# Optimization experiments

Measured on AMD Instinct MI355X. Metric: run time of the kernel, lower is better.

The kernel has to match this reference:

```python
import jax, jax.numpy as jnp
import numpy as np

N_GRAPHS = 100
BN_EPS = 1e-5
L = 4


def batch_norm(x, gamma, beta):
    # torch BatchNorm1d in training mode: biased batch statistics over the node dim
    mu = jnp.mean(x, axis=0)
    var = jnp.var(x, axis=0)
    return gamma * (x - mu) * jax.lax.rsqrt(var + BN_EPS) + beta


def setup_inputs() -> dict:
    key = jax.random.key(0)
    ks = jax.random.split(key, 24)
    N, E, IN, H, C = 50000, 600000, 128, 128, 10
    s = 0.05
    inp = {
        "h": jax.random.normal(ks[0], (N, IN), jnp.float32),
        "snorm_n": jax.random.uniform(ks[1], (N, 1), jnp.float32),
        "edge_src": jax.random.randint(ks[2], (E,), 0, N, jnp.int32),
        "edge_dst": jax.random.randint(ks[3], (E,), 0, N, jnp.int32),
        "graph_ids": jnp.sort(jax.random.randint(ks[4], (N,), 0, N_GRAPHS, jnp.int32)),
        # embedding_h
        "emb_W": jax.random.normal(ks[5], (IN, H), jnp.float32) * s,
        "emb_b": jnp.zeros((H,), jnp.float32),
        # per-layer GIN params, stacked over L layers
        "eps": jnp.zeros((L,), jnp.float32),
        "W1": jax.random.normal(ks[6], (L, H, H), jnp.float32) * s,
        "b1": jnp.zeros((L, H), jnp.float32),
        "g1": jnp.ones((L, H), jnp.float32),   # MLP internal BN gamma
        "be1": jnp.zeros((L, H), jnp.float32),  # MLP internal BN beta
        "W2": jax.random.normal(ks[7], (L, H, H), jnp.float32) * s,
        "b2": jnp.zeros((L, H), jnp.float32),
        "ga": jnp.ones((L, H), jnp.float32),    # ApplyNodeFunc BN gamma
        "ba": jnp.zeros((L, H), jnp.float32),
        "gl": jnp.ones((L, H), jnp.float32),    # GINLayer node BN gamma
        "bl": jnp.zeros((L, H), jnp.float32),
        # linears_prediction (L+1 of them)
        "pred_W": jax.random.normal(ks[8], (L + 1, H, C), jnp.float32) * s,
        "pred_b": jnp.zeros((L + 1, C), jnp.float32),
    }
    return inp


def reference(h, snorm_n, edge_src, edge_dst, graph_ids, emb_W, emb_b, eps,
              W1, b1, g1, be1, W2, b2, ga, ba, gl, bl, pred_W, pred_b):
    N = h.shape[0]
    h = h @ emb_W + emb_b  # embedding_h
    hidden_rep = [h]
    for i in range(L):
        h_in = h
        # sum-aggregate neighbor features (irregular gather + scatter-add)
        neigh = jax.ops.segment_sum(h[edge_src], edge_dst, num_segments=N)
        z = (1.0 + eps[i]) * h + neigh
        # ApplyNodeFunc: MLP (lin->BN->relu->lin) then BN then relu
        z = jax.nn.relu(batch_norm(z @ W1[i] + b1[i], g1[i], be1[i]))
        z = z @ W2[i] + b2[i]
        z = jax.nn.relu(batch_norm(z, ga[i], ba[i]))
        z = z * snorm_n                      # graph_norm
        z = batch_norm(z, gl[i], bl[i])      # batch_norm
        z = jax.nn.relu(z)
        h = h_in + z                         # residual (dropout p=0)
        hidden_rep.append(h)
    score = jnp.zeros((N_GRAPHS, pred_W.shape[-1]), h.dtype)
    for i, hr in enumerate(hidden_rep):
        pooled = jax.ops.segment_sum(hr, graph_ids, num_segments=N_GRAPHS)
        score = score + pooled @ pred_W[i] + pred_b[i]
    return score
```

## Files before the change

### kernel.cpp

```cpp
#include <hip/hip_runtime.h>

#define HD __device__ __forceinline__

static constexpr int H = 128;
static constexpr int G = 100;
static constexpr int L = 4;
static constexpr int C = 10;
static constexpr int DEGCAP = 64;

typedef __attribute__((ext_vector_type(8))) short short8;
typedef __attribute__((ext_vector_type(4))) float f32x4;

HD float bf2f(unsigned int u16) {
    return __uint_as_float(u16 << 16);
}
HD unsigned int f2bf(float f) {
    unsigned int u = __float_as_uint(f);
    u += 0x7fffu + ((u >> 16) & 1u);
    return u >> 16;
}

__global__ __launch_bounds__(256) void wprep_kernel(const float* __restrict__ embW,
                                                    const float* __restrict__ W1,
                                                    const float* __restrict__ W2,
                                                    unsigned short* __restrict__ WT,
                                                    unsigned short* __restrict__ Hb) {
    int mat = blockIdx.y;
    if (mat == 0 && blockIdx.x == 0 && threadIdx.x < 64)
        ((unsigned int*)Hb)[threadIdx.x] = 0u;
    const float* src = (mat == 0) ? embW
                     : (mat <= L) ? W1 + (size_t)(mat - 1) * H * H
                                  : W2 + (size_t)(mat - 1 - L) * H * H;
    int t = blockIdx.x * 256 + threadIdx.x;
    int col = t >> 7, k = t & 127;
    WT[(size_t)mat * H * H + col * H + k] = (unsigned short)f2bf(src[(size_t)k * H + col]);
}

__global__ void fill_kernel(const int* __restrict__ src, const int* __restrict__ dst, int E,
                            int* __restrict__ cnt, int* __restrict__ esrc) {
    int e = blockIdx.x * blockDim.x + threadIdx.x;
    if (e < E) {
        int d = dst[e];
        int pos = atomicAdd(&cnt[d], 1) & (DEGCAP - 1);
        esrc[(size_t)d * DEGCAP + pos] = src[e] + 1;
    }
}

__global__ __launch_bounds__(256) void agg_kernel(const unsigned short* __restrict__ HbZ,
                                                  const int* __restrict__ cnt,
                                                  const int* __restrict__ esrc,
                                                  const float* __restrict__ eps, int layer,
                                                  unsigned short* __restrict__ ZB, int N) {
    int node = blockIdx.x * 4 + (threadIdx.x >> 6);
    int lane = threadIdx.x & 63;
    if (node >= N) return;
    const unsigned int* H2 = (const unsigned int*)HbZ;
    float e1 = 1.0f + eps[layer];
    unsigned int hv = H2[(size_t)(node + 1) * 64 + lane];
    float ax = e1 * bf2f(hv & 0xffffu);
    float ay = e1 * bf2f(hv >> 16);
    int deg = min(cnt[node], DEGCAP);
    int degPad = min((deg + 15) & ~15, DEGCAP);
    const int* ep = esrc + (size_t)node * DEGCAP;
    for (int j = 0; j < degPad; j += 16) {
        unsigned int v[16];
#pragma unroll
        for (int u = 0; u < 16; ++u) v[u] = H2[(size_t)ep[j + u] * 64 + lane];
        float sx[4] = {0.f, 0.f, 0.f, 0.f}, sy[4] = {0.f, 0.f, 0.f, 0.f};
#pragma unroll
        for (int u = 0; u < 16; ++u) {
            sx[u & 3] += bf2f(v[u] & 0xffffu);
            sy[u & 3] += bf2f(v[u] >> 16);
        }
        ax += (sx[0] + sx[1]) + (sx[2] + sx[3]);
        ay += (sy[0] + sy[1]) + (sy[2] + sy[3]);
    }
    ((unsigned int*)ZB)[(size_t)node * 64 + lane] = f2bf(ax) | (f2bf(ay) << 16);
}

template <bool ABF16, bool TRANS, bool STATS, bool POOLF, bool HOFF>
__global__ __launch_bounds__(256, 4) void mgemm_kernel(
    const float* __restrict__ Af, const unsigned short* __restrict__ Ab,
    const unsigned short* __restrict__ WT, const float* __restrict__ bias,
    const float* __restrict__ sum_in, const float* __restrict__ sq_in,
    const float* __restrict__ gam, const float* __restrict__ bet, float invN,
    unsigned short* __restrict__ outB,
    int N, float* __restrict__ sum_out, float* __restrict__ sq_out,
    const int* __restrict__ gids, float* __restrict__ pool) {
    __shared__ unsigned short As[64 * 136];
    __shared__ float cas[H], ccs[H];
    int tid = threadIdx.x;
    int w = tid >> 6, lane = tid & 63, q = lane >> 4, m = lane & 15;
    int row0 = blockIdx.x * 64;
    int colbase = w * 32;

    short8 bfrag[2][4];
#pragma unroll
    for (int nt = 0; nt < 2; ++nt) {
        const unsigned short* wc = WT + (size_t)(colbase + nt * 16 + m) * H;
#pragma unroll
        for (int kk = 0; kk < 4; ++kk)
            bfrag[nt][kk] = *(const short8*)&wc[kk * 32 + q * 8];
    }

    if (TRANS) {
        if (tid < H) {
            float mu = sum_in[tid] * invN;
            float var = sq_in[tid] * invN - mu * mu;
            float inv = rsqrtf(var + 1e-5f);
            float a = gam[tid] * inv;
            cas[tid] = a;
            ccs[tid] = bet[tid] - mu * a;
        }
        __syncthreads();
    }

    {
        int cc = tid & 15, rg = tid >> 4;
        int c0 = cc * 8;
        float a8[8], b8[8];
        if (TRANS) {
#pragma unroll
            for (int j = 0; j < 8; ++j) { a8[j] = cas[c0 + j]; b8[j] = ccs[c0 + j]; }
        }
#pragma unroll
        for (int rr = 0; rr < 4; ++rr) {
            int r = rg * 4 + rr;
            int gr = row0 + r;
            uint4 o = {0u, 0u, 0u, 0u};
            if (ABF16 && !TRANS) {
                if (gr < N) o = *(const uint4*)&Ab[(size_t)gr * H + c0];
            } else {
                float v[8] = {0.f, 0.f, 0.f, 0.f, 0.f, 0.f, 0.f, 0.f};
                if (gr < N) {
                    if (ABF16) {
                        uint4 x = *(const uint4*)&Ab[(size_t)gr * H + c0];
                        v[0] = bf2f(x.x & 0xffffu); v[1] = bf2f(x.x >> 16);
                        v[2] = bf2f(x.y & 0xffffu); v[3] = bf2f(x.y >> 16);
                        v[4] = bf2f(x.z & 0xffffu); v[5] = bf2f(x.z >> 16);
                        v[6] = bf2f(x.w & 0xffffu); v[7] = bf2f(x.w >> 16);
                    } else {
                        float4 x0 = *(const float4*)&Af[(size_t)gr * H + c0];
                        float4 x1 = *(const float4*)&Af[(size_t)gr * H + c0 + 4];
                        v[0] = x0.x; v[1] = x0.y; v[2] = x0.z; v[3] = x0.w;
                        v[4] = x1.x; v[5] = x1.y; v[6] = x1.z; v[7] = x1.w;
                    }
                }
                if (TRANS) {
#pragma unroll
                    for (int j = 0; j < 8; ++j) v[j] = fmaxf(a8[j] * v[j] + b8[j], 0.f);
                }
                o.x = f2bf(v[0]) | (f2bf(v[1]) << 16);
                o.y = f2bf(v[2]) | (f2bf(v[3]) << 16);
                o.z = f2bf(v[4]) | (f2bf(v[5]) << 16);
                o.w = f2bf(v[6]) | (f2bf(v[7]) << 16);
            }
            *(uint4*)&As[r * 136 + c0] = o;
        }
    }
    __syncthreads();

    f32x4 acc[4][2];
#pragma unroll
    for (int mt = 0; mt < 4; ++mt)
#pragma unroll
        for (int nt = 0; nt < 2; ++nt) acc[mt][nt] = (f32x4){0.f, 0.f, 0.f, 0.f};
#pragma unroll
    for (int kk = 0; kk < 4; ++kk) {
        short8 af[4];
#pragma unroll
        for (int mt = 0; mt < 4; ++mt)
            af[mt] = *(const short8*)&As[(mt * 16 + m) * 136 + kk * 32 + q * 8];
#pragma unroll
        for (int mt = 0; mt < 4; ++mt)
#pragma unroll
            for (int nt = 0; nt < 2; ++nt)
                acc[mt][nt] = __builtin_amdgcn_mfma_f32_16x16x32_bf16(
                    af[mt], bfrag[nt][kk], acc[mt][nt], 0, 0, 0);
    }

    float bs2[2] = {bias[colbase + m], bias[colbase + 16 + m]};
    float s[2] = {0.f, 0.f}, qq[2] = {0.f, 0.f};
#pragma unroll
    for (int mt = 0; mt < 4; ++mt)
#pragma unroll
        for (int nt = 0; nt < 2; ++nt) {
            int gcol = colbase + nt * 16 + m;
#pragma unroll
            for (int rg = 0; rg < 4; ++rg) {
                int grow = row0 + mt * 16 + q * 4 + rg;
                float v = acc[mt][nt][rg] + bs2[nt];
                if (grow < N) {
                    outB[(size_t)(HOFF ? grow + 1 : grow) * H + gcol] = (unsigned short)f2bf(v);
                    if (STATS || POOLF) {
                        s[nt] += v;
                        if (STATS) qq[nt] += v * v;
                    }
                }
            }
        }

    if (STATS) {
#pragma unroll
        for (int nt = 0; nt < 2; ++nt) {
            float sv = s[nt], qv = qq[nt];
            sv += __shfl_xor(sv, 16); sv += __shfl_xor(sv, 32);
            qv += __shfl_xor(qv, 16); qv += __shfl_xor(qv, 32);
            if (q == 0) {
                atomicAdd(&sum_out[colbase + nt * 16 + m], sv);
                atomicAdd(&sq_out[colbase + nt * 16 + m], qv);
            }
        }
    }

    if (POOLF) {
        int last = min(row0 + 63, N - 1);
        bool uni = (gids[row0] == gids[last]);
        if (uni) {
            int g = gids[row0];
#pragma unroll
            for (int nt = 0; nt < 2; ++nt) {
                float sv = s[nt];
                sv += __shfl_xor(sv, 16); sv += __shfl_xor(sv, 32);
                if (q == 0) atomicAdd(&pool[g * H + colbase + nt * 16 + m], sv);
            }
        } else {
#pragma unroll
            for (int mt = 0; mt < 4; ++mt)
#pragma unroll
                for (int nt = 0; nt < 2; ++nt)
#pragma unroll
                    for (int rg = 0; rg < 4; ++rg) {
                        int grow = row0 + mt * 16 + q * 4 + rg;
                        if (grow < N) {
                            float v = acc[mt][nt][rg] + bs2[nt];
                            atomicAdd(&pool[gids[grow] * H + colbase + nt * 16 + m], v);
                        }
                    }
        }
    }
}

__global__ __launch_bounds__(256) void statsv_kernel(const unsigned short* __restrict__ UB,
                                                     const float* __restrict__ snorm,
                                                     const float* __restrict__ sum2, const float* __restrict__ sq2,
                                                     const float* __restrict__ ga, const float* __restrict__ ba,
                                                     float invN, int N,
                                                     float* __restrict__ sum3, float* __restrict__ sq3) {
    __shared__ float cas[H], ccs[H];
    int t = threadIdx.x;
    if (t < H) {
        float m = sum2[t] * invN;
        float var = sq2[t] * invN - m * m;
        float inv = rsqrtf(var + 1e-5f);
        float a = ga[t] * inv;
        cas[t] = a;
        ccs[t] = ba[t] - m * a;
    }
    __syncthreads();
    int col2 = t & 63, part = t >> 6;
    int c0 = col2 * 2, c1 = c0 + 1;
    float a0 = cas[c0], b0 = ccs[c0], a1 = cas[c1], b1 = ccs[c1];
    float s0 = 0.f, q0 = 0.f, s1 = 0.f, q1 = 0.f;
    const unsigned int* U2 = (const unsigned int*)UB;
    for (int r = blockIdx.x * 4 + part; r < N; r += gridDim.x * 4) {
        float sn = snorm[r];
        unsigned int v = U2[(size_t)r * 64 + col2];
        float v0 = fmaxf(a0 * bf2f(v & 0xffffu) + b0, 0.f) * sn;
        float v1 = fmaxf(a1 * bf2f(v >> 16) + b1, 0.f) * sn;
        s0 += v0; q0 += v0 * v0;
        s1 += v1; q1 += v1 * v1;
    }
    __shared__ float S[4][H], Q[4][H];
    S[part][c0] = s0; S[part][c1] = s1;
    Q[part][c0] = q0; Q[part][c1] = q1;
    __syncthreads();
    if (t < H) {
        atomicAdd(&sum3[t], S[0][t] + S[1][t] + S[2][t] + S[3][t]);
        atomicAdd(&sq3[t], Q[0][t] + Q[1][t] + Q[2][t] + Q[3][t]);
    }
}

__global__ __launch_bounds__(256) void tail_kernel(unsigned short* __restrict__ HbZ,
                                                   const unsigned short* __restrict__ UB,
                                                   const float* __restrict__ snorm,
                                                   const float* __restrict__ sum2, const float* __restrict__ sq2,
                                                   const float* __restrict__ ga, const float* __restrict__ ba,
                                                   const float* __restrict__ sum3, const float* __restrict__ sq3,
                                                   const float* __restrict__ gl, const float* __restrict__ bl,
                                                   float invN, const int* __restrict__ gids,
                                                   float* __restrict__ pool, int N) {
    __shared__ float ca2[H], cc2[H], ca3[H], cc3[H];
    __shared__ float PS[8][H];
    int t = threadIdx.x;
    if (t < H) {
        float m2 = sum2[t] * invN, v2 = sq2[t] * invN - m2 * m2;
        float i2 = rsqrtf(v2 + 1e-5f), a2 = ga[t] * i2;
        ca2[t] = a2; cc2[t] = ba[t] - m2 * a2;
        float m3 = sum3[t] * invN, v3 = sq3[t] * invN - m3 * m3;
        float i3 = rsqrtf(v3 + 1e-5f), a3 = gl[t] * i3;
        ca3[t] = a3; cc3[t] = bl[t] - m3 * a3;
    }
    __syncthreads();
    int row0 = blockIdx.x * 32;
    int col4 = t & 31, rowg = t >> 5;
    int c0 = col4 * 4;
    float A2[4], B2[4], A3[4], B3[4];
#pragma unroll
    for (int j = 0; j < 4; ++j) {
        A2[j] = ca2[c0 + j]; B2[j] = cc2[c0 + j];
        A3[j] = ca3[c0 + j]; B3[j] = cc3[c0 + j];
    }
    bool uni = (gids[row0] == gids[min(row0 + 31, N - 1)]);
    float p[4] = {0.f, 0.f, 0.f, 0.f};
    const uint2* U4 = (const uint2*)UB;
    uint2* H4 = (uint2*)HbZ;
#pragma unroll
    for (int rr = 0; rr < 4; ++rr) {
        int r = row0 + rowg * 4 + rr;
        if (r < N) {
            float sn = snorm[r];
            uint2 uv = U4[(size_t)r * 32 + col4];
            uint2 hv = H4[(size_t)(r + 1) * 32 + col4];
            float u[4] = {bf2f(uv.x & 0xffffu), bf2f(uv.x >> 16), bf2f(uv.y & 0xffffu), bf2f(uv.y >> 16)};
            float h[4] = {bf2f(hv.x & 0xffffu), bf2f(hv.x >> 16), bf2f(hv.y & 0xffffu), bf2f(hv.y >> 16)};
#pragma unroll
            for (int j = 0; j < 4; ++j) {
                float v = fmaxf(A2[j] * u[j] + B2[j], 0.f) * sn;
                h[j] += fmaxf(A3[j] * v + B3[j], 0.f);
            }
            uint2 hb;
            hb.x = f2bf(h[0]) | (f2bf(h[1]) << 16);
            hb.y = f2bf(h[2]) | (f2bf(h[3]) << 16);
            H4[(size_t)(r + 1) * 32 + col4] = hb;
            if (uni) {
                p[0] += h[0]; p[1] += h[1]; p[2] += h[2]; p[3] += h[3];
            } else {
                int g = gids[r];
#pragma unroll
                for (int j = 0; j < 4; ++j) atomicAdd(&pool[g * H + c0 + j], h[j]);
            }
        }
    }
    if (uni) {
#pragma unroll
        for (int j = 0; j < 4; ++j) PS[rowg][c0 + j] = p[j];
        __syncthreads();
        if (t < H) {
            float s = PS[0][t] + PS[1][t] + PS[2][t] + PS[3][t] +
                      PS[4][t] + PS[5][t] + PS[6][t] + PS[7][t];
            atomicAdd(&pool[gids[row0] * H + t], s);
        }
    }
}

__global__ void final_kernel(const float* __restrict__ pool, const float* __restrict__ pw,
                             const float* __restrict__ pb, float* __restrict__ out) {
    int g = blockIdx.x, t = threadIdx.x;
    __shared__ float p[H];
    float acc = 0.f;
    for (int i = 0; i <= L; ++i) {
        p[t] = pool[(size_t)(i * G + g) * H + t];
        __syncthreads();
        if (t < C) {
            float s = 0.f;
            for (int f = 0; f < H; ++f) s += p[f] * pw[(size_t)(i * H + f) * C + t];
            acc += s + pb[i * C + t];
        }
        __syncthreads();
    }
    if (t < C) out[g * C + t] = acc;
}

extern "C" void kernel_launch(void* const* d_in, const int* in_sizes, int n_in,
                              void* d_out, int out_size, void* d_ws, size_t ws_size,
                              hipStream_t stream) {
    const float* h_in  = (const float*)d_in[0];
    const float* snorm = (const float*)d_in[1];
    const int* esrc_in = (const int*)d_in[2];
    const int* edst_in = (const int*)d_in[3];
    const int* gids    = (const int*)d_in[4];
    const float* embW = (const float*)d_in[5];
    const float* embB = (const float*)d_in[6];
    const float* eps  = (const float*)d_in[7];
    const float* W1   = (const float*)d_in[8];
    const float* b1   = (const float*)d_in[9];
    const float* g1   = (const float*)d_in[10];
    const float* be1  = (const float*)d_in[11];
    const float* W2   = (const float*)d_in[12];
    const float* b2   = (const float*)d_in[13];
    const float* ga   = (const float*)d_in[14];
    const float* ba   = (const float*)d_in[15];
    const float* gl   = (const float*)d_in[16];
    const float* bl   = (const float*)d_in[17];
    const float* predW = (const float*)d_in[18];
    const float* predB = (const float*)d_in[19];

    const int N = in_sizes[0] / H;
    const int E = in_sizes[2];
    const float invN = 1.0f / (float)N;

    float* ws = (float*)d_ws;
    float* POOL = ws;
    float* STATS = POOL + (size_t)(L + 1) * G * H;
    int* CNT = (int*)(STATS + (size_t)L * 6 * H);
    int* ESRC = CNT + N;
    unsigned short* WT = (unsigned short*)(ESRC + (size_t)N * DEGCAP);
    unsigned short* Hb = WT + (size_t)9 * H * H;
    unsigned short* ZB = Hb + (size_t)(N + 1) * H;
    unsigned short* TB = ZB + (size_t)N * H;
    unsigned short* UB = ZB;

    size_t zbytes = ((size_t)(L + 1) * G * H + (size_t)L * 6 * H + N + (size_t)N * DEGCAP) * 4;
    hipMemsetAsync(POOL, 0, zbytes, stream);

    wprep_kernel<<<dim3(64, 9), 256, 0, stream>>>(embW, W1, W2, WT, Hb);
    fill_kernel<<<(E + 255) / 256, 256, 0, stream>>>(esrc_in, edst_in, E, CNT, ESRC);

    int gblocks = (N + 63) / 64;
    mgemm_kernel<false, false, false, true, true><<<gblocks, 256, 0, stream>>>(
        h_in, nullptr, WT, embB, nullptr, nullptr, nullptr, nullptr, invN,
        Hb, N, nullptr, nullptr, gids, POOL);

    for (int i = 0; i < L; ++i) {
        float* S1 = STATS + (size_t)i * 6 * H;
        float* Q1 = S1 + H;
        float* S2 = Q1 + H;
        float* Q2 = S2 + H;
        float* S3 = Q2 + H;
        float* Q3 = S3 + H;
        agg_kernel<<<(N + 3) / 4, 256, 0, stream>>>(Hb, CNT, ESRC, eps, i, ZB, N);
        mgemm_kernel<true, false, true, false, false><<<gblocks, 256, 0, stream>>>(
            nullptr, ZB, WT + (size_t)(1 + i) * H * H, b1 + (size_t)i * H,
            nullptr, nullptr, nullptr, nullptr, invN,
            TB, N, S1, Q1, nullptr, nullptr);
        mgemm_kernel<true, true, true, false, false><<<gblocks, 256, 0, stream>>>(
            nullptr, TB, WT + (size_t)(1 + L + i) * H * H, b2 + (size_t)i * H,
            S1, Q1, g1 + (size_t)i * H, be1 + (size_t)i * H, invN,
            UB, N, S2, Q2, nullptr, nullptr);
        statsv_kernel<<<256, 256, 0, stream>>>(UB, snorm, S2, Q2,
                                               ga + (size_t)i * H, ba + (size_t)i * H, invN, N, S3, Q3);
        tail_kernel<<<(N + 31) / 32, 256, 0, stream>>>(Hb, UB, snorm,
                                                       S2, Q2, ga + (size_t)i * H, ba + (size_t)i * H,
                                                       S3, Q3, gl + (size_t)i * H, bl + (size_t)i * H,
                                                       invN, gids, POOL + (size_t)(i + 1) * G * H, N);
    }
    final_kernel<<<G, H, 0, stream>>>(POOL, predW, predB, (float*)d_out);
}
```

Baseline: 698.1 us.

## Fuse stats and tail kernels with a grid barrier; merge prep kernels

Merges the weight-prep and edge-fill kernels into one launch, and fuses the per-layer statistics pass with the tail pass into a single persistent kernel of 512 blocks. The two phases are separated by a software grid-wide barrier built on an atomic counter that lives in the zeroed workspace. This removes several launches per layer and lets the tail reuse block-resident state. The barrier only works if all 512 blocks are co-resident, which is the purpose of the launch bound of 2 blocks per CU, and the spin-wait adds some synchronisation cost.

```diff
diff --git a/kernel.cpp b/kernel.cpp
--- a/kernel.cpp
+++ b/kernel.cpp
@@ -20,29 +20,30 @@
     return u >> 16;
 }
 
-__global__ __launch_bounds__(256) void wprep_kernel(const float* __restrict__ embW,
-                                                    const float* __restrict__ W1,
-                                                    const float* __restrict__ W2,
-                                                    unsigned short* __restrict__ WT,
-                                                    unsigned short* __restrict__ Hb) {
-    int mat = blockIdx.y;
-    if (mat == 0 && blockIdx.x == 0 && threadIdx.x < 64)
-        ((unsigned int*)Hb)[threadIdx.x] = 0u;
-    const float* src = (mat == 0) ? embW
-                     : (mat <= L) ? W1 + (size_t)(mat - 1) * H * H
-                                  : W2 + (size_t)(mat - 1 - L) * H * H;
-    int t = blockIdx.x * 256 + threadIdx.x;
-    int col = t >> 7, k = t & 127;
-    WT[(size_t)mat * H * H + col * H + k] = (unsigned short)f2bf(src[(size_t)k * H + col]);
-}
-
-__global__ void fill_kernel(const int* __restrict__ src, const int* __restrict__ dst, int E,
-                            int* __restrict__ cnt, int* __restrict__ esrc) {
-    int e = blockIdx.x * blockDim.x + threadIdx.x;
-    if (e < E) {
-        int d = dst[e];
-        int pos = atomicAdd(&cnt[d], 1) & (DEGCAP - 1);
-        esrc[(size_t)d * DEGCAP + pos] = src[e] + 1;
+__global__ __launch_bounds__(256) void prep_kernel(
+    const float* __restrict__ embW, const float* __restrict__ W1, const float* __restrict__ W2,
+    unsigned short* __restrict__ WT, unsigned short* __restrict__ Hb,
+    const int* __restrict__ src, const int* __restrict__ dst, int E,
+    int* __restrict__ cnt, int* __restrict__ esrc) {
+    int b = blockIdx.x;
+    if (b < 576) {
+        int mat = b >> 6;
+        int bx = b & 63;
+        if (b == 0 && threadIdx.x < 64)
+            ((unsigned int*)Hb)[threadIdx.x] = 0u;
+        const float* s = (mat == 0) ? embW
+                       : (mat <= L) ? W1 + (size_t)(mat - 1) * H * H
+                                    : W2 + (size_t)(mat - 1 - L) * H * H;
+        int t = bx * 256 + threadIdx.x;
+        int col = t >> 7, k = t & 127;
+        WT[(size_t)mat * H * H + col * H + k] = (unsigned short)f2bf(s[(size_t)k * H + col]);
+    } else {
+        int e = (b - 576) * 256 + threadIdx.x;
+        if (e < E) {
+            int d = dst[e];
+            int pos = atomicAdd(&cnt[d], 1) & (DEGCAP - 1);
+            esrc[(size_t)d * DEGCAP + pos] = src[e] + 1;
+        }
     }
 }
 
@@ -241,115 +242,123 @@
     }
 }
 
-__global__ __launch_bounds__(256) void statsv_kernel(const unsigned short* __restrict__ UB,
-                                                     const float* __restrict__ snorm,
-                                                     const float* __restrict__ sum2, const float* __restrict__ sq2,
-                                                     const float* __restrict__ ga, const float* __restrict__ ba,
-                                                     float invN, int N,
-                                                     float* __restrict__ sum3, float* __restrict__ sq3) {
-    __shared__ float cas[H], ccs[H];
+__global__ __launch_bounds__(256, 2) void stv_tail_kernel(
+    unsigned short* __restrict__ HbZ, const unsigned short* __restrict__ UB,
+    const float* __restrict__ snorm,
+    const float* __restrict__ S2, const float* __restrict__ Q2,
+    const float* __restrict__ ga, const float* __restrict__ ba,
+    float* __restrict__ S3, float* __restrict__ Q3,
+    const float* __restrict__ gl, const float* __restrict__ bl,
+    float invN, const int* __restrict__ gids, float* __restrict__ pool,
+    int N, int* __restrict__ bar) {
+    __shared__ float c1[H], c2[H], c3[H], c4[H];
+    __shared__ float SS[4][H], QQ[4][H];
     int t = threadIdx.x;
+
     if (t < H) {
-        float m = sum2[t] * invN;
-        float var = sq2[t] * invN - m * m;
+        float mu = S2[t] * invN;
+        float var = Q2[t] * invN - mu * mu;
         float inv = rsqrtf(var + 1e-5f);
         float a = ga[t] * inv;
-        cas[t] = a;
-        ccs[t] = ba[t] - m * a;
+        c1[t] = a;
+        c2[t] = ba[t] - mu * a;
     }
     __syncthreads();
-    int col2 = t & 63, part = t >> 6;
-    int c0 = col2 * 2, c1 = c0 + 1;
-    float a0 = cas[c0], b0 = ccs[c0], a1 = cas[c1], b1 = ccs[c1];
-    float s0 = 0.f, q0 = 0.f, s1 = 0.f, q1 = 0.f;
-    const unsigned int* U2 = (const unsigned int*)UB;
-    for (int r = blockIdx.x * 4 + part; r < N; r += gridDim.x * 4) {
-        float sn = snorm[r];
-        unsigned int v = U2[(size_t)r * 64 + col2];
-        float v0 = fmaxf(a0 * bf2f(v & 0xffffu) + b0, 0.f) * sn;
-        float v1 = fmaxf(a1 * bf2f(v >> 16) + b1, 0.f) * sn;
-        s0 += v0; q0 += v0 * v0;
-        s1 += v1; q1 += v1 * v1;
-    }
-    __shared__ float S[4][H], Q[4][H];
-    S[part][c0] = s0; S[part][c1] = s1;
-    Q[part][c0] = q0; Q[part][c1] = q1;
+    {
+        int col2 = t & 63, part = t >> 6;
+        int cA = col2 * 2, cB = cA + 1;
+        float a0 = c1[cA], b0 = c2[cA], a1 = c1[cB], b1 = c2[cB];
+        float s0 = 0.f, q0 = 0.f, s1 = 0.f, q1 = 0.f;
+        const unsigned int* U2 = (const unsigned int*)UB;
+        for (int r = blockIdx.x * 4 + part; r < N; r += gridDim.x * 4) {
+            float sn = snorm[r];
+            unsigned int v = U2[(size_t)r * 64 + col2];
+            float v0 = fmaxf(a0 * bf2f(v & 0xffffu) + b0, 0.f) * sn;
+            float v1 = fmaxf(a1 * bf2f(v >> 16) + b1, 0.f) * sn;
+            s0 += v0; q0 += v0 * v0;
+            s1 += v1; q1 += v1 * v1;
+        }
+        SS[part][cA] = s0; SS[part][cB] = s1;
+        QQ[part][cA] = q0; QQ[part][cB] = q1;
+        __syncthreads();
+        if (t < H) {
+            atomicAdd(&S3[t], SS[0][t] + SS[1][t] + SS[2][t] + SS[3][t]);
+            atomicAdd(&Q3[t], QQ[0][t] + QQ[1][t] + QQ[2][t] + QQ[3][t]);
+        }
+        __syncthreads();
+    }
+
+    if (t == 0) {
+        __threadfence();
+        atomicAdd(bar, 1);
+        while (__hip_atomic_load(bar, __ATOMIC_RELAXED, __HIP_MEMORY_SCOPE_AGENT) < (int)gridDim.x)
+            __builtin_amdgcn_s_sleep(2);
+    }
     __syncthreads();
+    __threadfence();
+
     if (t < H) {
-        atomicAdd(&sum3[t], S[0][t] + S[1][t] + S[2][t] + S[3][t]);
-        atomicAdd(&sq3[t], Q[0][t] + Q[1][t] + Q[2][t] + Q[3][t]);
-    }
-}
-
-__global__ __launch_bounds__(256) void tail_kernel(unsigned short* __restrict__ HbZ,
-                                                   const unsigned short* __restrict__ UB,
-                                                   const float* __restrict__ snorm,
-                                                   const float* __restrict__ sum2, const float* __restrict__ sq2,
-                                                   const float* __restrict__ ga, const float* __restrict__ ba,
-                                                   const float* __restrict__ sum3, const float* __restrict__ sq3,
-                                                   const float* __restrict__ gl, const float* __restrict__ bl,
-                                                   float invN, const int* __restrict__ gids,
-                                                   float* __restrict__ pool, int N) {
-    __shared__ float ca2[H], cc2[H], ca3[H], cc3[H];
-    __shared__ float PS[8][H];
-    int t = threadIdx.x;
-    if (t < H) {
-        float m2 = sum2[t] * invN, v2 = sq2[t] * invN - m2 * m2;
-        float i2 = rsqrtf(v2 + 1e-5f), a2 = ga[t] * i2;
-        ca2[t] = a2; cc2[t] = ba[t] - m2 * a2;
-        float m3 = sum3[t] * invN, v3 = sq3[t] * invN - m3 * m3;
+        float m3 = S3[t] * invN, v3 = Q3[t] * invN - m3 * m3;
         float i3 = rsqrtf(v3 + 1e-5f), a3 = gl[t] * i3;
-        ca3[t] = a3; cc3[t] = bl[t] - m3 * a3;
+        c3[t] = a3;
+        c4[t] = bl[t] - m3 * a3;
     }
     __syncthreads();
-    int row0 = blockIdx.x * 32;
+    float* PS = &SS[0][0];
     int col4 = t & 31, rowg = t >> 5;
     int c0 = col4 * 4;
     float A2[4], B2[4], A3[4], B3[4];
 #pragma unroll
     for (int j = 0; j < 4; ++j) {
-        A2[j] = ca2[c0 + j]; B2[j] = cc2[c0 + j];
-        A3[j] = ca3[c0 + j]; B3[j] = cc3[c0 + j];
-    }
-    bool uni = (gids[row0] == gids[min(row0 + 31, N - 1)]);
-    float p[4] = {0.f, 0.f, 0.f, 0.f};
+        A2[j] = c1[c0 + j]; B2[j] = c2[c0 + j];
+        A3[j] = c3[c0 + j]; B3[j] = c4[c0 + j];
+    }
     const uint2* U4 = (const uint2*)UB;
     uint2* H4 = (uint2*)HbZ;
-#pragma unroll
-    for (int rr = 0; rr < 4; ++rr) {
-        int r = row0 + rowg * 4 + rr;
-        if (r < N) {
-            float sn = snorm[r];
-            uint2 uv = U4[(size_t)r * 32 + col4];
-            uint2 hv = H4[(size_t)(r + 1) * 32 + col4];
-            float u[4] = {bf2f(uv.x & 0xffffu), bf2f(uv.x >> 16), bf2f(uv.y & 0xffffu), bf2f(uv.y >> 16)};
-            float h[4] = {bf2f(hv.x & 0xffffu), bf2f(hv.x >> 16), bf2f(hv.y & 0xffffu), bf2f(hv.y >> 16)};
-#pragma unroll
-            for (int j = 0; j < 4; ++j) {
-                float v = fmaxf(A2[j] * u[j] + B2[j], 0.f) * sn;
-                h[j] += fmaxf(A3[j] * v + B3[j], 0.f);
-            }
-            uint2 hb;
-            hb.x = f2bf(h[0]) | (f2bf(h[1]) << 16);
-            hb.y = f2bf(h[2]) | (f2bf(h[3]) << 16);
-            H4[(size_t)(r + 1) * 32 + col4] = hb;
-            if (uni) {
-                p[0] += h[0]; p[1] += h[1]; p[2] += h[2]; p[3] += h[3];
-            } else {
-                int g = gids[r];
-#pragma unroll
-                for (int j = 0; j < 4; ++j) atomicAdd(&pool[g * H + c0 + j], h[j]);
-            }
-        }
-    }
-    if (uni) {
-#pragma unroll
-        for (int j = 0; j < 4; ++j) PS[rowg][c0 + j] = p[j];
-        __syncthreads();
-        if (t < H) {
-            float s = PS[0][t] + PS[1][t] + PS[2][t] + PS[3][t] +
-                      PS[4][t] + PS[5][t] + PS[6][t] + PS[7][t];
-            atomicAdd(&pool[gids[row0] * H + t], s);
+    int tiles32 = (N + 31) / 32;
+    for (int t32 = blockIdx.x; t32 < tiles32; t32 += gridDim.x) {
+        int row0 = t32 * 32;
+        bool uni = (gids[row0] == gids[min(row0 + 31, N - 1)]);
+        float p[4] = {0.f, 0.f, 0.f, 0.f};
+#pragma unroll
+        for (int rr = 0; rr < 4; ++rr) {
+            int r = row0 + rowg * 4 + rr;
+            if (r < N) {
+                float sn = snorm[r];
+                uint2 uv = U4[(size_t)r * 32 + col4];
+                uint2 hv = H4[(size_t)(r + 1) * 32 + col4];
+                float u[4] = {bf2f(uv.x & 0xffffu), bf2f(uv.x >> 16),
+                              bf2f(uv.y & 0xffffu), bf2f(uv.y >> 16)};
+                float h[4] = {bf2f(hv.x & 0xffffu), bf2f(hv.x >> 16),
+                              bf2f(hv.y & 0xffffu), bf2f(hv.y >> 16)};
+#pragma unroll
+                for (int j = 0; j < 4; ++j) {
+                    float v = fmaxf(A2[j] * u[j] + B2[j], 0.f) * sn;
+                    h[j] += fmaxf(A3[j] * v + B3[j], 0.f);
+                }
+                uint2 hb;
+                hb.x = f2bf(h[0]) | (f2bf(h[1]) << 16);
+                hb.y = f2bf(h[2]) | (f2bf(h[3]) << 16);
+                H4[(size_t)(r + 1) * 32 + col4] = hb;
+                if (uni) {
+                    p[0] += h[0]; p[1] += h[1]; p[2] += h[2]; p[3] += h[3];
+                } else {
+                    int g = gids[r];
+#pragma unroll
+                    for (int j = 0; j < 4; ++j) atomicAdd(&pool[g * H + c0 + j], h[j]);
+                }
+            }
+        }
+        if (uni) {
+#pragma unroll
+            for (int j = 0; j < 4; ++j) PS[rowg * H + c0 + j] = p[j];
+            __syncthreads();
+            if (t < H) {
+                float s = PS[t] + PS[H + t] + PS[2 * H + t] + PS[3 * H + t] +
+                          PS[4 * H + t] + PS[5 * H + t] + PS[6 * H + t] + PS[7 * H + t];
+                atomicAdd(&pool[gids[row0] * H + t], s);
+            }
+            __syncthreads();
         }
     }
 }
@@ -403,7 +412,8 @@
     float* ws = (float*)d_ws;
     float* POOL = ws;
     float* STATS = POOL + (size_t)(L + 1) * G * H;
-    int* CNT = (int*)(STATS + (size_t)L * 6 * H);
+    int* BAR = (int*)(STATS + (size_t)L * 6 * H);
+    int* CNT = BAR + 16;
     int* ESRC = CNT + N;
     unsigned short* WT = (unsigned short*)(ESRC + (size_t)N * DEGCAP);
     unsigned short* Hb = WT + (size_t)9 * H * H;
@@ -411,11 +421,12 @@
     unsigned short* TB = ZB + (size_t)N * H;
     unsigned short* UB = ZB;
 
-    size_t zbytes = ((size_t)(L + 1) * G * H + (size_t)L * 6 * H + N + (size_t)N * DEGCAP) * 4;
+    size_t zbytes = ((size_t)(L + 1) * G * H + (size_t)L * 6 * H + 16 + N + (size_t)N * DEGCAP) * 4;
     hipMemsetAsync(POOL, 0, zbytes, stream);
 
-    wprep_kernel<<<dim3(64, 9), 256, 0, stream>>>(embW, W1, W2, WT, Hb);
-    fill_kernel<<<(E + 255) / 256, 256, 0, stream>>>(esrc_in, edst_in, E, CNT, ESRC);
+    int prep_blocks = 576 + (E + 255) / 256;
+    prep_kernel<<<prep_blocks, 256, 0, stream>>>(embW, W1, W2, WT, Hb,
+                                                 esrc_in, edst_in, E, CNT, ESRC);
 
     int gblocks = (N + 63) / 64;
     mgemm_kernel<false, false, false, true, true><<<gblocks, 256, 0, stream>>>(
@@ -438,12 +449,11 @@
             nullptr, TB, WT + (size_t)(1 + L + i) * H * H, b2 + (size_t)i * H,
             S1, Q1, g1 + (size_t)i * H, be1 + (size_t)i * H, invN,
             UB, N, S2, Q2, nullptr, nullptr);
-        statsv_kernel<<<256, 256, 0, stream>>>(UB, snorm, S2, Q2,
-                                               ga + (size_t)i * H, ba + (size_t)i * H, invN, N, S3, Q3);
-        tail_kernel<<<(N + 31) / 32, 256, 0, stream>>>(Hb, UB, snorm,
-                                                       S2, Q2, ga + (size_t)i * H, ba + (size_t)i * H,
-                                                       S3, Q3, gl + (size_t)i * H, bl + (size_t)i * H,
-                                                       invN, gids, POOL + (size_t)(i + 1) * G * H, N);
+        stv_tail_kernel<<<512, 256, 0, stream>>>(Hb, UB, snorm, S2, Q2,
+                                                 ga + (size_t)i * H, ba + (size_t)i * H,
+                                                 S3, Q3, gl + (size_t)i * H, bl + (size_t)i * H,
+                                                 invN, gids, POOL + (size_t)(i + 1) * G * H,
+                                                 N, BAR + i);
     }
     final_kernel<<<G, H, 0, stream>>>(POOL, predW, predB, (float*)d_out);
 }
```

Result: slower. 894.4 us (+28.1%).
